# Optimization experiments

Measured on AMD Instinct MI355X. Metric: run time of the kernel, lower is better.

## Reference

```python
import jax, jax.numpy as jnp
import numpy as np
from jax import lax


def setup_inputs() -> dict:
    key = jax.random.key(0)
    kx, kw = jax.random.split(key)
    x = jax.random.normal(kx, (32, 3, 8192), dtype=jnp.float32)
    weight = jax.random.normal(kw, (128, 3, 64), dtype=jnp.float32)
    return {"x": x, "weight": weight}


def reference(x, weight):
    # x: [B, C, L], weight: [O, C, K]
    K = weight.shape[2]
    # Cross-correlation (conv1d, no bias, valid padding): [B, O, L-K+1]
    conv_out = lax.conv_general_dilated(
        x, weight, window_strides=(1,), padding='VALID',
        dimension_numbers=('NCH', 'OIH', 'NCH'))
    # Half squared norm of each shapelet: [O]
    w_norm = jnp.sum(weight ** 2, axis=(1, 2)) / 2
    # Half squared norm of each length-K window, via cumulative sums
    # (avoids materializing the [B, C, W, K] unfold tensor)
    sq = jnp.sum(x ** 2, axis=1)               # [B, L]
    c = jnp.pad(jnp.cumsum(sq, axis=1), ((0, 0), (1, 0)))  # [B, L+1]
    win_norm = (c[:, K:] - c[:, :-K]) / 2      # [B, L-K+1]
    # features = conv_out - (||w||^2/2 + ||window||^2/2)
    features = conv_out - w_norm[None, :, None] - win_norm[:, None, :]
    # global max-pool over time, then *(-2) -> min squared distance
    return -2.0 * jnp.max(features, axis=-1)   # [B, O]
```

## Files before the change

kernel.cpp:

```cpp
#include <hip/hip_runtime.h>
#include <float.h>

#define BB 32
#define LL 8192
#define OO 128
#define KK 64
#define WW (LL - KK + 1)
#define NCH 4
#define GX 8

typedef __attribute__((ext_vector_type(8))) short short8;
typedef __attribute__((ext_vector_type(4))) float f32x4;

union AB { int4 i4; int i[4]; short8 v; };

static __device__ __forceinline__ unsigned int f2bf(float f) {
    unsigned int u = __builtin_bit_cast(unsigned int, f);
    return (u + 0x7FFFu + ((u >> 16) & 1u)) >> 16;
}

__global__ __launch_bounds__(256) void prep_kernel(const float* __restrict__ w,
                                                   unsigned short* __restrict__ wswz,
                                                   float* __restrict__ wn) {
    int g = blockIdx.x * 256 + threadIdx.x;
    if (g < 3072) {
        int ob = (g >= 1536) ? 1 : 0;
        int gg = g - ob * 1536;
        int ksqp = gg >> 6;
        int o2   = gg & 63;
        int ks = ksqp >> 2, qp = ksqp & 3;
        int c = ks >> 1, h = ks & 1;
        const float4* p = (const float4*)(w + (ob * 64 + o2) * 192 + c * 64 + h * 32 + qp * 8);
        float4 v0 = p[0], v1 = p[1];
        int4 pk;
        pk.x = (int)(f2bf(v0.x) | (f2bf(v0.y) << 16));
        pk.y = (int)(f2bf(v0.z) | (f2bf(v0.w) << 16));
        pk.z = (int)(f2bf(v1.x) | (f2bf(v1.y) << 16));
        pk.w = (int)(f2bf(v1.z) | (f2bf(v1.w) << 16));
        ((int4*)wswz)[g] = pk;
    }
    int oo = g - 3072;
    if (oo >= 0 && oo < OO) {
        const float* p = w + oo * 192;
        float s = 0.f;
        for (int i = 0; i < 192; ++i) { float v = p[i]; s = fmaf(v, v, s); }
        wn[oo] = 0.5f * s;
    }
}

static __device__ __forceinline__ void stage_chunk(const float* __restrict__ x, int b, int T0,
                                                   unsigned short* xl, float* sql, float* Pl,
                                                   int tid) {
    if (tid < 240) {
        int c = tid / 80, j4 = tid - c * 80;
        int l = T0 + j4 * 4;
        float4 v = make_float4(0.f, 0.f, 0.f, 0.f);
        if (l < LL) v = *(const float4*)(x + (b * 3 + c) * LL + l);
        uint2 pk;
        pk.x = f2bf(v.x) | (f2bf(v.y) << 16);
        pk.y = f2bf(v.z) | (f2bf(v.w) << 16);
        *(uint2*)(xl + c * 320 + j4 * 4) = pk;
    }
    {
        int l = T0 + tid;
        float s = 0.f;
        if (l < LL) {
            #pragma unroll
            for (int c = 0; c < 3; ++c) {
                float v = x[(b * 3 + c) * LL + l];
                s = fmaf(v, v, s);
            }
        }
        sql[tid] = s;
        float s8 = s + __shfl_xor(s, 1, 64);
        s8 += __shfl_xor(s8, 2, 64);
        s8 += __shfl_xor(s8, 4, 64);
        if ((tid & 7) == 0) Pl[tid >> 3] = s8;
    }
    if (tid < 64) {
        int j = 256 + tid, l = T0 + j;
        float s = 0.f;
        if (l < LL) {
            #pragma unroll
            for (int c = 0; c < 3; ++c) {
                float v = x[(b * 3 + c) * LL + l];
                s = fmaf(v, v, s);
            }
        }
        sql[j] = s;
        float s8 = s + __shfl_xor(s, 1, 64);
        s8 += __shfl_xor(s8, 2, 64);
        s8 += __shfl_xor(s8, 4, 64);
        if ((tid & 7) == 0) Pl[32 + (tid >> 3)] = s8;
    }
}

__global__ __launch_bounds__(256, 2) void shapeconv_main(const float* __restrict__ x,
                                                         const unsigned short* __restrict__ wswz,
                                                         const float* __restrict__ wn,
                                                         float* __restrict__ partial) {
    __shared__ __align__(16) unsigned short w_lds[64 * 192];
    __shared__ __align__(16) unsigned short x_lds[2][3 * 320];
    __shared__ __align__(16) float sq_lds[2][320];
    __shared__ float P_lds[2][40];
    __shared__ float win_lds[272];
    __shared__ float wn_lds[64];
    __shared__ float mred[64];

    const int tcx = blockIdx.x;
    const int ob = blockIdx.y;
    const int b  = blockIdx.z;
    const int tid = threadIdx.x;
    const int wv = tid >> 6;
    const int lane = tid & 63;
    const int wo = wv & 1, wt = wv >> 1;
    const int n  = lane & 15;
    const int qp = lane >> 4;
    const int Tb = tcx * (NCH * 256);

    {
        const char* src = (const char*)(wswz + ob * 1536 * 8) + tid * 16;
        #pragma unroll
        for (int i = 0; i < 6; ++i) {
            __builtin_amdgcn_global_load_lds(
                (const __attribute__((address_space(1))) unsigned int*)(src + i * 4096),
                (__attribute__((address_space(3))) unsigned int*)((char*)w_lds + wv * 1024 + i * 4096),
                16, 0, 0);
        }
    }
    if (tid < 64) wn_lds[tid] = wn[ob * 64 + tid];

    stage_chunk(x, b, Tb, x_lds[0], sq_lds[0], P_lds[0], tid);

    float m2[2][4];
    #pragma unroll
    for (int ot = 0; ot < 2; ++ot)
        #pragma unroll
        for (int rg = 0; rg < 4; ++rg) m2[ot][rg] = -FLT_MAX;

    for (int ci = 0; ci < NCH; ++ci) {
        const int bsel = ci & 1;
        const int T0 = Tb + ci * 256;
        __syncthreads();

        {
            int a = tid >> 3, bb2 = tid & 7;
            const float* sql = sq_lds[bsel];
            const float* Pl = P_lds[bsel];
            float s = 0.f;
            #pragma unroll
            for (int i = 1; i <= 7; ++i) s += Pl[a + i];
            #pragma unroll
            for (int k = 0; k < 8; ++k)
                s += (k >= bb2) ? sql[8 * a + k] : sql[8 * a + 64 + k];
            int pi = tid + (tid >> 4);
            win_lds[pi] = (T0 + tid < WW) ? 0.5f * s : 1e30f;
        }
        __syncthreads();

        f32x4 acc[2][8];
        {
            float wl[8];
            #pragma unroll
            for (int r = 0; r < 8; ++r) {
                int tl = 128 * wt + r + 8 * n;
                wl[r] = win_lds[tl + (tl >> 4)];
            }
            #pragma unroll
            for (int ot = 0; ot < 2; ++ot)
                #pragma unroll
                for (int rg = 0; rg < 4; ++rg) {
                    float nw = wn_lds[32 * wo + 16 * ot + 4 * qp + rg];
                    #pragma unroll
                    for (int r = 0; r < 8; ++r)
                        acc[ot][r][rg] = -nw - wl[r];
                }
        }

        if (ci + 1 < NCH)
            stage_chunk(x, b, T0 + 256, x_lds[1 - bsel], sq_lds[1 - bsel], P_lds[1 - bsel], tid);

        const char* xb = (const char*)x_lds[bsel];
        #pragma unroll
        for (int ks = 0; ks < 6; ++ks) {
            int c = ks >> 1, h = ks & 1;
            int e0b = c * 640 + 256 * wt + 64 * h + 16 * (n + qp);
            int4 Ea = *(const int4*)(xb + e0b);
            int4 Eb = *(const int4*)(xb + e0b + 16);
            int D[8] = {Ea.x, Ea.y, Ea.z, Ea.w, Eb.x, Eb.y, Eb.z, Eb.w};
            AB a0, a1;
            const int4* wq = (const int4*)w_lds + (ks * 4 + qp) * 64 + 32 * wo;
            a0.i4 = wq[n];
            a1.i4 = wq[16 + n];
            #pragma unroll
            for (int r = 0; r < 8; ++r) {
                AB bf;
                int s = r >> 1;
                if ((r & 1) == 0) {
                    bf.i[0] = D[s]; bf.i[1] = D[s + 1]; bf.i[2] = D[s + 2]; bf.i[3] = D[s + 3];
                } else {
                    #pragma unroll
                    for (int d = 0; d < 4; ++d)
                        bf.i[d] = (int)(((unsigned)D[s + d] >> 16) | ((unsigned)D[s + d + 1] << 16));
                }
                acc[0][r] = __builtin_amdgcn_mfma_f32_16x16x32_bf16(a0.v, bf.v, acc[0][r], 0, 0, 0);
                acc[1][r] = __builtin_amdgcn_mfma_f32_16x16x32_bf16(a1.v, bf.v, acc[1][r], 0, 0, 0);
            }
        }

        #pragma unroll
        for (int ot = 0; ot < 2; ++ot)
            #pragma unroll
            for (int rg = 0; rg < 4; ++rg) {
                float mm = m2[ot][rg];
                #pragma unroll
                for (int r = 0; r < 8; ++r) mm = fmaxf(mm, acc[ot][r][rg]);
                m2[ot][rg] = mm;
            }
    }

    #pragma unroll
    for (int s = 1; s <= 8; s <<= 1)
        #pragma unroll
        for (int ot = 0; ot < 2; ++ot)
            #pragma unroll
            for (int rg = 0; rg < 4; ++rg)
                m2[ot][rg] = fmaxf(m2[ot][rg], __shfl_xor(m2[ot][rg], s, 64));

    if (wt == 1 && n == 0) {
        #pragma unroll
        for (int ot = 0; ot < 2; ++ot)
            #pragma unroll
            for (int rg = 0; rg < 4; ++rg)
                mred[32 * wo + 16 * ot + 4 * qp + rg] = m2[ot][rg];
    }
    __syncthreads();
    if (wt == 0 && n == 0) {
        #pragma unroll
        for (int ot = 0; ot < 2; ++ot)
            #pragma unroll
            for (int rg = 0; rg < 4; ++rg) {
                int oi = 32 * wo + 16 * ot + 4 * qp + rg;
                float v = fmaxf(m2[ot][rg], mred[oi]);
                partial[((size_t)(b * GX + tcx) * 2 + ob) * 64 + oi] = v;
            }
    }
}

__global__ __launch_bounds__(256) void reduce_kernel(const float* __restrict__ partial,
                                                     float* __restrict__ out) {
    int idx = blockIdx.x * 256 + threadIdx.x;
    int b = idx >> 7, o = idx & 127;
    const float* pp = partial + ((size_t)b * GX * 2 + (o >> 6)) * 64 + (o & 63);
    float mx = -FLT_MAX;
    #pragma unroll
    for (int t = 0; t < GX; ++t) mx = fmaxf(mx, pp[(size_t)t * 128]);
    out[idx] = -2.f * mx;
}

extern "C" void kernel_launch(void* const* d_in, const int* in_sizes, int n_in,
                              void* d_out, int out_size, void* d_ws, size_t ws_size,
                              hipStream_t stream) {
    const float* x = (const float*)d_in[0];
    const float* w = (const float*)d_in[1];
    float* out = (float*)d_out;

    unsigned short* wswz = (unsigned short*)d_ws;
    float* wn = (float*)((char*)d_ws + 49152);
    float* partial = (float*)((char*)d_ws + 49664);

    prep_kernel<<<13, 256, 0, stream>>>(w, wswz, wn);
    dim3 grid(GX, 2, BB);
    shapeconv_main<<<grid, 256, 0, stream>>>(x, wswz, wn, partial);
    reduce_kernel<<<16, 256, 0, stream>>>(partial, out);
}
```

Measured before the change: 74.45 us.

## Keep weight fragments in registers and compute window norms per lane

Weight MFMA A-fragments and shapelet norms are loaded once from global memory into registers instead of being staged in LDS. Each lane now computes its own eight window norms with a sliding sum, which removes the win_lds buffer and one __syncthreads per chunk. The chunk loop is also fully unrolled. This cuts LDS traffic and barriers, and the smaller LDS footprint may allow more resident blocks, at the cost of higher VGPR pressure (48 extra registers for the fragments) that could limit occupancy.

```diff
diff --git a/kernel.cpp b/kernel.cpp
--- a/kernel.cpp
+++ b/kernel.cpp
@@ -99,12 +99,9 @@
                                                          const unsigned short* __restrict__ wswz,
                                                          const float* __restrict__ wn,
                                                          float* __restrict__ partial) {
-    __shared__ __align__(16) unsigned short w_lds[64 * 192];
     __shared__ __align__(16) unsigned short x_lds[2][3 * 320];
     __shared__ __align__(16) float sq_lds[2][320];
     __shared__ float P_lds[2][40];
-    __shared__ float win_lds[272];
-    __shared__ float wn_lds[64];
     __shared__ float mred[64];
 
     const int tcx = blockIdx.x;
@@ -118,17 +115,19 @@
     const int qp = lane >> 4;
     const int Tb = tcx * (NCH * 256);
 
-    {
-        const char* src = (const char*)(wswz + ob * 1536 * 8) + tid * 16;
-        #pragma unroll
-        for (int i = 0; i < 6; ++i) {
-            __builtin_amdgcn_global_load_lds(
-                (const __attribute__((address_space(1))) unsigned int*)(src + i * 4096),
-                (__attribute__((address_space(3))) unsigned int*)((char*)w_lds + wv * 1024 + i * 4096),
-                16, 0, 0);
-        }
-    }
-    if (tid < 64) wn_lds[tid] = wn[ob * 64 + tid];
+    AB afr[2][6];
+    #pragma unroll
+    for (int ot = 0; ot < 2; ++ot)
+        #pragma unroll
+        for (int ks = 0; ks < 6; ++ks)
+            afr[ot][ks].i4 = ((const int4*)wswz)[ob * 1536 + (ks * 4 + qp) * 64 + 32 * wo + 16 * ot + n];
+
+    float wnv[2][4];
+    #pragma unroll
+    for (int ot = 0; ot < 2; ++ot)
+        #pragma unroll
+        for (int rg = 0; rg < 4; ++rg)
+            wnv[ot][rg] = wn[ob * 64 + 32 * wo + 16 * ot + 4 * qp + rg];
 
     stage_chunk(x, b, Tb, x_lds[0], sq_lds[0], P_lds[0], tid);
 
@@ -138,60 +137,56 @@
         #pragma unroll
         for (int rg = 0; rg < 4; ++rg) m2[ot][rg] = -FLT_MAX;
 
+    #pragma unroll
     for (int ci = 0; ci < NCH; ++ci) {
         const int bsel = ci & 1;
         const int T0 = Tb + ci * 256;
         __syncthreads();
 
-        {
-            int a = tid >> 3, bb2 = tid & 7;
-            const float* sql = sq_lds[bsel];
-            const float* Pl = P_lds[bsel];
-            float s = 0.f;
-            #pragma unroll
-            for (int i = 1; i <= 7; ++i) s += Pl[a + i];
-            #pragma unroll
-            for (int k = 0; k < 8; ++k)
-                s += (k >= bb2) ? sql[8 * a + k] : sql[8 * a + 64 + k];
-            int pi = tid + (tid >> 4);
-            win_lds[pi] = (T0 + tid < WW) ? 0.5f * s : 1e30f;
-        }
-        __syncthreads();
-
-        f32x4 acc[2][8];
-        {
-            float wl[8];
-            #pragma unroll
-            for (int r = 0; r < 8; ++r) {
-                int tl = 128 * wt + r + 8 * n;
-                wl[r] = win_lds[tl + (tl >> 4)];
-            }
-            #pragma unroll
-            for (int ot = 0; ot < 2; ++ot)
-                #pragma unroll
-                for (int rg = 0; rg < 4; ++rg) {
-                    float nw = wn_lds[32 * wo + 16 * ot + 4 * qp + rg];
-                    #pragma unroll
-                    for (int r = 0; r < 8; ++r)
-                        acc[ot][r][rg] = -nw - wl[r];
-                }
-        }
-
         if (ci + 1 < NCH)
             stage_chunk(x, b, T0 + 256, x_lds[1 - bsel], sq_lds[1 - bsel], P_lds[1 - bsel], tid);
 
+        float wlm[8];
+        {
+            const float* sql = sq_lds[bsel];
+            const float* Pl  = P_lds[bsel];
+            int a = 16 * wt + n;
+            float4 H0 = *(const float4*)(sql + 8 * a);
+            float4 H1 = *(const float4*)(sql + 8 * a + 4);
+            float4 G0 = *(const float4*)(sql + 8 * a + 64);
+            float4 G1 = *(const float4*)(sql + 8 * a + 68);
+            float h[8] = {H0.x, H0.y, H0.z, H0.w, H1.x, H1.y, H1.z, H1.w};
+            float g[8] = {G0.x, G0.y, G0.z, G0.w, G1.x, G1.y, G1.z, G1.w};
+            float s = 0.f;
+            #pragma unroll
+            for (int i = 1; i <= 7; ++i) s += Pl[a + i];
+            #pragma unroll
+            for (int j = 0; j < 8; ++j) s += h[j];
+            int tg0 = T0 + 8 * a;
+            #pragma unroll
+            for (int r = 0; r < 8; ++r) {
+                wlm[r] = (tg0 + r < WW) ? 0.5f * s : 1e30f;
+                s = s - h[r] + g[r];
+            }
+        }
+
+        f32x4 acc[2][8];
+        #pragma unroll
+        for (int ot = 0; ot < 2; ++ot)
+            #pragma unroll
+            for (int rg = 0; rg < 4; ++rg)
+                #pragma unroll
+                for (int r = 0; r < 8; ++r)
+                    acc[ot][r][rg] = -wnv[ot][rg] - wlm[r];
+
         const char* xb = (const char*)x_lds[bsel];
         #pragma unroll
         for (int ks = 0; ks < 6; ++ks) {
-            int c = ks >> 1, h = ks & 1;
-            int e0b = c * 640 + 256 * wt + 64 * h + 16 * (n + qp);
+            int c = ks >> 1, h2 = ks & 1;
+            int e0b = c * 640 + 256 * wt + 64 * h2 + 16 * (n + qp);
             int4 Ea = *(const int4*)(xb + e0b);
             int4 Eb = *(const int4*)(xb + e0b + 16);
             int D[8] = {Ea.x, Ea.y, Ea.z, Ea.w, Eb.x, Eb.y, Eb.z, Eb.w};
-            AB a0, a1;
-            const int4* wq = (const int4*)w_lds + (ks * 4 + qp) * 64 + 32 * wo;
-            a0.i4 = wq[n];
-            a1.i4 = wq[16 + n];
             #pragma unroll
             for (int r = 0; r < 8; ++r) {
                 AB bf;
@@ -203,8 +198,8 @@
                     for (int d = 0; d < 4; ++d)
                         bf.i[d] = (int)(((unsigned)D[s + d] >> 16) | ((unsigned)D[s + d + 1] << 16));
                 }
-                acc[0][r] = __builtin_amdgcn_mfma_f32_16x16x32_bf16(a0.v, bf.v, acc[0][r], 0, 0, 0);
-                acc[1][r] = __builtin_amdgcn_mfma_f32_16x16x32_bf16(a1.v, bf.v, acc[1][r], 0, 0, 0);
+                acc[0][r] = __builtin_amdgcn_mfma_f32_16x16x32_bf16(afr[0][ks].v, bf.v, acc[0][r], 0, 0, 0);
+                acc[1][r] = __builtin_amdgcn_mfma_f32_16x16x32_bf16(afr[1][ks].v, bf.v, acc[1][r], 0, 0, 0);
             }
         }
 
```

Measured after the change: 76.08 us. +2.2%, slower.
